# Kernel optimization log

Hardware: AMD Instinct MI355X
Metric: run time of the kernel (lower is better)

## Reference

```python
import jax, jax.numpy as jnp
import numpy as np

B, S, HID = 2, 2048, 2048
H, HKV, D = 16, 8, 128
RQ, RK, RV = 6, 2, 2
WINDOW = 1024
SOFTCAP = 50.0
SCALING = D ** -0.5
NEG_INF = -2.3819763e38  # gemma mask fill value (fp32 safe)


def _rope(x, cos, sin):
    # Gemma rotary: split last dim into two halves treated as (real, imag).
    d2 = x.shape[-1] // 2
    x1, x2 = x[..., :d2], x[..., d2:]
    return jnp.concatenate([x1 * cos - x2 * sin, x1 * sin + x2 * cos], axis=-1)


def setup_inputs() -> dict:
    key = jax.random.key(0)
    ks = jax.random.split(key, 8)
    hidden_states = jax.random.normal(ks[0], (B, S, HID), jnp.float32)
    w = 0.02
    W_A_q = jax.random.normal(ks[1], (HID, H * RQ), jnp.float32) * w
    W_B_q = jax.random.normal(ks[2], (HID, H * RQ * D), jnp.float32) * w
    W_A_k = jax.random.normal(ks[3], (HID, HKV * RK), jnp.float32) * w
    W_B_k = jax.random.normal(ks[4], (HID, RK * D), jnp.float32) * w
    W_A_v = jax.random.normal(ks[5], (HID, HKV * RV), jnp.float32) * w
    W_B_v = jax.random.normal(ks[6], (HID, RV * D), jnp.float32) * w
    W_o = jax.random.normal(ks[7], (H * D, HID), jnp.float32) * w
    # rotary tables (theta=10000)
    pos = jnp.arange(S, dtype=jnp.float32)
    inv = 1.0 / (10000.0 ** (jnp.arange(0, D, 2, dtype=jnp.float32) / D))
    ang = pos[:, None] * inv[None, :]  # [S, D/2]
    freqs_cos, freqs_sin = jnp.cos(ang), jnp.sin(ang)
    # causal + sliding-window additive mask [B,1,S,S]
    i = jnp.arange(S)[:, None]
    j = jnp.arange(S)[None, :]
    allowed = (j <= i) & (i - j < WINDOW)
    mask = jnp.where(allowed, 0.0, NEG_INF).astype(jnp.float32)
    mask = jnp.broadcast_to(mask[None, None], (B, 1, S, S))
    kv_write_indices = jnp.arange(S, dtype=jnp.int32)  # prefill: identity write
    return {
        'hidden_states': hidden_states, 'W_A_q': W_A_q, 'W_B_q': W_B_q,
        'W_A_k': W_A_k, 'W_B_k': W_B_k, 'W_A_v': W_A_v, 'W_B_v': W_B_v,
        'W_o': W_o, 'freqs_cos': freqs_cos, 'freqs_sin': freqs_sin,
        'mask': mask, 'kv_write_indices': kv_write_indices,
    }


def reference(hidden_states, W_A_q, W_B_q, W_A_k, W_B_k, W_A_v, W_B_v, W_o,
              freqs_cos, freqs_sin, mask, kv_write_indices):
    # Prefill: kv_write_indices == arange(S); factorized cache == current factors.
    b, s, _ = hidden_states.shape
    Aq = (hidden_states @ W_A_q).reshape(b, s, H, RQ)       # [b,s,H,Rq]
    Bq = (hidden_states @ W_B_q).reshape(b, s, H, RQ, D)    # [b,s,H,Rq,d]
    Ak = (hidden_states @ W_A_k).reshape(b, s, HKV, RK)
    Bk = (hidden_states @ W_B_k).reshape(b, s, RK, D)
    Av = (hidden_states @ W_A_v).reshape(b, s, HKV, RV)
    Bv = (hidden_states @ W_B_v).reshape(b, s, RV, D)
    # RoPE on the B factors (as in the original: applied to B_q rows and B_k rows)
    Bq = _rope(Bq, freqs_cos[:, None, None, :], freqs_sin[:, None, None, :])
    Bk = _rope(Bk, freqs_cos[:, None, :], freqs_sin[:, None, :])
    # Contract rank factors. Identical math to the per-head
    # einsum('bqrd,bksd->bqkrs') + einsum('bqr,bks,bqkrs->bqk') since the
    # bilinear form factorizes: sum_{r,s} Aq_r Ak_s <Bq_r, Bk_s> = <q, k>.
    q = jnp.einsum('bshr,bshrd->bshd', Aq, Bq)               # [b,s,H,d]
    k = jnp.einsum('bsgr,bsrd->bsgd', Ak, Bk)                # [b,s,Hkv,d]
    v = jnp.einsum('bsgr,bsrd->bsgd', Av, Bv)
    rep = H // HKV
    k = jnp.repeat(k, rep, axis=2)                            # GQA expand
    v = jnp.repeat(v, rep, axis=2)
    scores = jnp.einsum('bqhd,bkhd->bhqk', q, k) * SCALING
    scores = jnp.tanh(scores / SOFTCAP) * SOFTCAP             # logit softcap
    scores = scores + mask                                    # local sliding mask
    probs = jax.nn.softmax(scores, axis=-1)
    out = jnp.einsum('bhqk,bkhd->bqhd', probs, v).reshape(b, s, H * D)
    return out @ W_o
```

## Files before the change

kernel.cpp:

```cpp
#include <hip/hip_runtime.h>
#include <hip/hip_bf16.h>

#define S_LEN 2048
#define HID 2048
#define NB 2
#define NH 16
#define NKV 8
#define DH 128
#define RQ 6
#define KG 2048
#define SCALING 0.08838834764831845f

typedef __attribute__((ext_vector_type(8))) short s16x8;
typedef __attribute__((ext_vector_type(4))) float f32x4;

__device__ __forceinline__ float bf2f(ushort u) {
    union { unsigned int i; float f; } v; v.i = ((unsigned int)u) << 16; return v.f;
}
__device__ __forceinline__ ushort f2bf(float f) {
    __hip_bfloat16 h = __float2bfloat16(f);
    return *reinterpret_cast<ushort*>(&h);
}
__device__ __forceinline__ void g2lds16(const void* g, void* l) {
    __builtin_amdgcn_global_load_lds((const __attribute__((address_space(1))) void*)g,
                                     (__attribute__((address_space(3))) void*)l, 16, 0, 0);
}

__global__ void k_cvt_bf16(const float* __restrict__ in, ushort* __restrict__ out, int n4) {
    int i = blockIdx.x * 256 + threadIdx.x;
    if (i >= n4) return;
    float4 v = ((const float4*)in)[i];
    ushort4 o;
    o.x = f2bf(v.x); o.y = f2bf(v.y); o.z = f2bf(v.z); o.w = f2bf(v.w);
    ((ushort4*)out)[i] = o;
}

__global__ void k_transpose_w(const float* __restrict__ in, ushort* __restrict__ out, int Nin, int rowOff) {
    __shared__ ushort tile[64][66];
    int k0 = blockIdx.x * 64, n0 = blockIdx.y * 64;
    int t = threadIdx.x;
#pragma unroll
    for (int i = 0; i < 16; ++i) {
        int f = t + i * 256; int r = f >> 6, c = f & 63;
        int nn = n0 + c;
        float v = (nn < Nin) ? in[(size_t)(k0 + r) * Nin + nn] : 0.f;
        tile[r][c] = f2bf(v);
    }
    __syncthreads();
#pragma unroll
    for (int i = 0; i < 16; ++i) {
        int f = t + i * 256; int nr = f >> 6, kc = f & 63;
        int nn = n0 + nr;
        if (nn < Nin) out[(size_t)(rowOff + nn) * KG + k0 + kc] = tile[kc][nr];
    }
}

__device__ __forceinline__ void stc(float* p, float v) { *p = v; }
__device__ __forceinline__ void stc(ushort* p, float v) { *p = f2bf(v); }

template<typename OutT>
__global__ __launch_bounds__(256, 2) void k_gemm(const ushort* __restrict__ A,
                                                 const ushort* __restrict__ Bt,
                                                 OutT* __restrict__ C, int ldc) {
    __shared__ ushort lA[128 * 64];
    __shared__ ushort lB[128 * 64];
    const int tid = threadIdx.x;
    const int l = tid & 63, w = tid >> 6;
    const int gx = gridDim.x;
    int flat = blockIdx.y * gx + blockIdx.x;
    const int nwg = gx * gridDim.y;
    if ((nwg & 7) == 0) {
        int qq = nwg >> 3;
        flat = (flat & 7) * qq + (flat >> 3);
    }
    const int m0 = (flat % gx) * 128, n0 = (flat / gx) * 128;
    const int wm = w >> 1, wn = w & 1;
    f32x4 acc[4][4] = {};
    const int swz = 16 * ((tid & 7) ^ ((tid >> 3) & 7));
    const int rowbase = tid >> 3;

    for (int k0 = 0; k0 < KG; k0 += 64) {
#pragma unroll
        for (int i = 0; i < 4; ++i) {
            int row = rowbase + i * 32;
            const char* srcA = (const char*)A + (((size_t)(m0 + row) * KG + k0) * 2) + swz;
            g2lds16(srcA, (char*)lA + tid * 16 + i * 4096);
            const char* srcB = (const char*)Bt + (((size_t)(n0 + row) * KG + k0) * 2) + swz;
            g2lds16(srcB, (char*)lB + tid * 16 + i * 4096);
        }
        __syncthreads();
#pragma unroll
        for (int kk = 0; kk < 2; ++kk) {
            s16x8 af[4], bfr[4];
            const int kb = kk * 64 + (l >> 4) * 16;
#pragma unroll
            for (int mf = 0; mf < 4; ++mf) {
                int row = wm * 64 + mf * 16 + (l & 15);
                af[mf] = *(const s16x8*)((const char*)lA + row * 128 + (kb ^ ((row & 7) << 4)));
            }
#pragma unroll
            for (int nf = 0; nf < 4; ++nf) {
                int row = wn * 64 + nf * 16 + (l & 15);
                bfr[nf] = *(const s16x8*)((const char*)lB + row * 128 + (kb ^ ((row & 7) << 4)));
            }
#pragma unroll
            for (int mf = 0; mf < 4; ++mf)
#pragma unroll
                for (int nf = 0; nf < 4; ++nf)
                    acc[mf][nf] = __builtin_amdgcn_mfma_f32_16x16x32_bf16(af[mf], bfr[nf], acc[mf][nf], 0, 0, 0);
        }
        __syncthreads();
    }
#pragma unroll
    for (int mf = 0; mf < 4; ++mf)
#pragma unroll
        for (int r = 0; r < 4; ++r) {
            int row = m0 + wm * 64 + mf * 16 + (l >> 4) * 4 + r;
#pragma unroll
            for (int nf = 0; nf < 4; ++nf) {
                int col = n0 + wn * 64 + nf * 16 + (l & 15);
                stc(C + (size_t)row * ldc + col, acc[mf][nf][r]);
            }
        }
}

__global__ __launch_bounds__(512, 2) void k_gemm8(const ushort* __restrict__ A,
                                                  const ushort* __restrict__ Bt,
                                                  ushort* __restrict__ C, int ldc) {
    __shared__ char sB[131072];
    const int tid = threadIdx.x;
    const int l = tid & 63, wid = tid >> 6;
    const int wr = wid >> 2, wc = wid & 3;

    int flat = blockIdx.x;
    const int nwg = gridDim.x;
    if ((nwg & 7) == 0) {
        int qq = nwg >> 3;
        flat = (flat & 7) * qq + (flat >> 3);
    }
    const int m0 = (flat & 15) * 256;
    const int n0 = (flat >> 4) * 256;

    const int rb = tid >> 3;
    const int swz = 16 * ((tid & 7) ^ (rb & 7));
    const char* pAh[2][2];
    const char* pBh[2][2];
#pragma unroll
    for (int h = 0; h < 2; ++h)
#pragma unroll
        for (int j = 0; j < 2; ++j) {
            pAh[h][j] = (const char*)A + (size_t)(m0 + j * 128 + h * 64 + rb) * (KG * 2) + swz;
            pBh[h][j] = (const char*)Bt + (size_t)(n0 + (j * 2 + (tid >> 8)) * 64 + h * 32 + (rb & 31)) * (KG * 2) + swz;
        }

    f32x4 acc[8][4] = {};
    s16x8 af[4][2], bf[4][2];

    const int arow = (l & 15) * 128;
    const int kxor0 = (0 * 64 + (l >> 4) * 16) ^ ((l & 7) << 4);
    const int kxor1 = (1 * 64 + (l >> 4) * 16) ^ ((l & 7) << 4);

#define STG_A(T, D, H)                                                                     \
    do {                                                                                   \
        g2lds16(pAh[H][0] + (size_t)(T) * 128, sB + (D) * 65536 + (H) * 16384 + tid * 16); \
        g2lds16(pAh[H][1] + (size_t)(T) * 128, sB + (D) * 65536 + (H) * 16384 + 8192 + tid * 16); \
    } while (0)
#define STG_B(T, D, H)                                                                     \
    do {                                                                                   \
        g2lds16(pBh[H][0] + (size_t)(T) * 128, sB + (D) * 65536 + 32768 + (H) * 16384 + tid * 16); \
        g2lds16(pBh[H][1] + (size_t)(T) * 128, sB + (D) * 65536 + 32768 + (H) * 16384 + 8192 + tid * 16); \
    } while (0)
#define RD_A(D, MH)                                                                        \
    do {                                                                                   \
        const char* ab = sB + (D) * 65536 + (MH) * 16384 + wr * 8192;                      \
        _Pragma("unroll") for (int mi = 0; mi < 4; ++mi) {                                 \
            af[mi][0] = *(const s16x8*)(ab + mi * 2048 + arow + kxor0);                    \
            af[mi][1] = *(const s16x8*)(ab + mi * 2048 + arow + kxor1);                    \
        }                                                                                  \
    } while (0)
#define RD_B(D, BH)                                                                        \
    do {                                                                                   \
        const char* bb = sB + (D) * 65536 + 32768 + (BH) * 16384 + wc * 4096;              \
        _Pragma("unroll") for (int ni = 0; ni < 2; ++ni) {                                 \
            bf[(BH) * 2 + ni][0] = *(const s16x8*)(bb + ni * 2048 + arow + kxor0);         \
            bf[(BH) * 2 + ni][1] = *(const s16x8*)(bb + ni * 2048 + arow + kxor1);         \
        }                                                                                  \
    } while (0)
#define QMFMA(MQ, NQ)                                                                      \
    do {                                                                                   \
        __builtin_amdgcn_s_setprio(1);                                                     \
        _Pragma("unroll") for (int mi = 0; mi < 4; ++mi)                                   \
        _Pragma("unroll") for (int ni = 0; ni < 2; ++ni)                                   \
        _Pragma("unroll") for (int k2 = 0; k2 < 2; ++k2)                                   \
            acc[(MQ) * 4 + mi][(NQ) * 2 + ni] = __builtin_amdgcn_mfma_f32_16x16x32_bf16(   \
                af[mi][k2], bf[(NQ) * 2 + ni][k2], acc[(MQ) * 4 + mi][(NQ) * 2 + ni], 0, 0, 0); \
        __builtin_amdgcn_s_setprio(0);                                                     \
    } while (0)
#define BAR()                                   \
    do {                                        \
        asm volatile("" ::: "memory");          \
        __builtin_amdgcn_s_barrier();           \
        asm volatile("" ::: "memory");          \
    } while (0)
#define VM6() asm volatile("s_waitcnt vmcnt(6)" ::: "memory")
#define VM0() asm volatile("s_waitcnt vmcnt(0)" ::: "memory")

    STG_A(0, 0, 0); STG_A(0, 0, 1); STG_B(0, 0, 0); STG_B(0, 0, 1);
    STG_B(1, 1, 0); STG_B(1, 1, 1); STG_A(1, 1, 0);
    VM6();
    BAR();

    for (int i = 0; i < 16; ++i) {
        const bool last = (i == 15);
        const int t1 = 2 * i + 1, t2 = 2 * i + 2, t3 = 2 * i + 3;
        RD_A(0, 0); RD_B(0, 0);
        STG_A(t1, 1, 1);
        BAR(); QMFMA(0, 0); BAR();
        RD_B(0, 1);
        if (!last) STG_A(t2, 0, 0);
        BAR(); QMFMA(0, 1); BAR();
        RD_A(0, 1);
        if (!last) STG_B(t2, 0, 0);
        BAR(); QMFMA(1, 1); BAR();
        if (!last) { STG_B(t2, 0, 1); VM6(); } else { VM0(); }
        BAR(); QMFMA(1, 0); BAR();
        RD_A(1, 0); RD_B(1, 0);
        if (!last) STG_A(t2, 0, 1);
        BAR(); QMFMA(0, 0); BAR();
        RD_B(1, 1);
        if (!last) STG_B(t3, 1, 0);
        BAR(); QMFMA(0, 1); BAR();
        RD_A(1, 1);
        if (!last) STG_B(t3, 1, 1);
        BAR(); QMFMA(1, 1); BAR();
        if (!last) { STG_A(t3, 1, 0); VM6(); }
        BAR(); QMFMA(1, 0); BAR();
    }

#undef STG_A
#undef STG_B
#undef RD_A
#undef RD_B
#undef QMFMA

#pragma unroll
    for (int mf = 0; mf < 8; ++mf)
#pragma unroll
        for (int r = 0; r < 4; ++r) {
            int row = m0 + wr * 128 + mf * 16 + (l >> 4) * 4 + r;
#pragma unroll
            for (int nf = 0; nf < 4; ++nf) {
                int col = n0 + wc * 64 + nf * 16 + (l & 15);
                C[(size_t)row * ldc + col] = f2bf(acc[mf][nf][r]);
            }
        }
#undef BAR
#undef VM6
#undef VM0
}

__global__ __launch_bounds__(512, 2) void k_gemm8h(const ushort* __restrict__ A,
                                                   const ushort* __restrict__ Bt,
                                                   float* __restrict__ C, int ldc) {
    __shared__ char sB[98304];
    const int tid = threadIdx.x;
    const int l = tid & 63, wid = tid >> 6;
    const int wr = wid >> 2, wc = wid & 3;

    int flat = blockIdx.x;
    const int nwg = gridDim.x;
    if ((nwg & 7) == 0) {
        int qq = nwg >> 3;
        flat = (flat & 7) * qq + (flat >> 3);
    }
    const int m0 = (flat & 31) * 128;
    const int n0 = (flat >> 5) * 256;

    const int rb = tid >> 3;
    const int swz = 16 * ((tid & 7) ^ (rb & 7));
    const char* pA_[2];
    const char* pB_[2][2];
#pragma unroll
    for (int h = 0; h < 2; ++h) {
        pA_[h] = (const char*)A + (size_t)(m0 + (tid >> 8) * 64 + h * 32 + (rb & 31)) * (KG * 2) + swz;
#pragma unroll
        for (int j = 0; j < 2; ++j)
            pB_[h][j] = (const char*)Bt + (size_t)(n0 + (j * 2 + (tid >> 8)) * 64 + h * 32 + (rb & 31)) * (KG * 2) + swz;
    }

    f32x4 acc[4][4] = {};
    s16x8 af[2][2], bf[4][2];

    const int arow = (l & 15) * 128;
    const int kxor0 = ((l >> 4) * 16) ^ ((l & 7) << 4);
    const int kxor1 = (64 + (l >> 4) * 16) ^ ((l & 7) << 4);

#define STG_AH(T, D, H)                                                                    \
    g2lds16(pA_[H] + (size_t)(T) * 128, sB + (D) * 49152 + (H) * 8192 + tid * 16)
#define STG_BH(T, D, H)                                                                    \
    do {                                                                                   \
        g2lds16(pB_[H][0] + (size_t)(T) * 128, sB + (D) * 49152 + 16384 + (H) * 16384 + tid * 16); \
        g2lds16(pB_[H][1] + (size_t)(T) * 128, sB + (D) * 49152 + 16384 + (H) * 16384 + 8192 + tid * 16); \
    } while (0)
#define RD_AH(D, MH)                                                                       \
    do {                                                                                   \
        const char* ab = sB + (D) * 49152 + (MH) * 8192 + wr * 4096;                       \
        _Pragma("unroll") for (int mi = 0; mi < 2; ++mi) {                                 \
            af[mi][0] = *(const s16x8*)(ab + mi * 2048 + arow + kxor0);                    \
            af[mi][1] = *(const s16x8*)(ab + mi * 2048 + arow + kxor1);                    \
        }                                                                                  \
    } while (0)
#define RD_BH(D, BH)                                                                       \
    do {                                                                                   \
        const char* bb = sB + (D) * 49152 + 16384 + (BH) * 16384 + wc * 4096;              \
        _Pragma("unroll") for (int ni = 0; ni < 2; ++ni) {                                 \
            bf[(BH) * 2 + ni][0] = *(const s16x8*)(bb + ni * 2048 + arow + kxor0);         \
            bf[(BH) * 2 + ni][1] = *(const s16x8*)(bb + ni * 2048 + arow + kxor1);         \
        }                                                                                  \
    } while (0)
#define QMFMAH(MQ, NQ)                                                                     \
    do {                                                                                   \
        __builtin_amdgcn_s_setprio(1);                                                     \
        _Pragma("unroll") for (int mi = 0; mi < 2; ++mi)                                   \
        _Pragma("unroll") for (int ni = 0; ni < 2; ++ni)                                   \
        _Pragma("unroll") for (int k2 = 0; k2 < 2; ++k2)                                   \
            acc[(MQ) * 2 + mi][(NQ) * 2 + ni] = __builtin_amdgcn_mfma_f32_16x16x32_bf16(   \
                af[mi][k2], bf[(NQ) * 2 + ni][k2], acc[(MQ) * 2 + mi][(NQ) * 2 + ni], 0, 0, 0); \
        __builtin_amdgcn_s_setprio(0);                                                     \
    } while (0)
#define BAR()                                   \
    do {                                        \
        asm volatile("" ::: "memory");          \
        __builtin_amdgcn_s_barrier();           \
        asm volatile("" ::: "memory");          \
    } while (0)
#define VM5() asm volatile("s_waitcnt vmcnt(5)" ::: "memory")
#define VM0() asm volatile("s_waitcnt vmcnt(0)" ::: "memory")

    STG_AH(0, 0, 0); STG_AH(0, 0, 1); STG_BH(0, 0, 0); STG_BH(0, 0, 1);
    STG_BH(1, 1, 0); STG_BH(1, 1, 1); STG_AH(1, 1, 0);
    VM5();
    BAR();

    for (int i = 0; i < 16; ++i) {
        const bool last = (i == 15);
        const int t1 = 2 * i + 1, t2 = 2 * i + 2, t3 = 2 * i + 3;
        RD_AH(0, 0); RD_BH(0, 0);
        STG_AH(t1, 1, 1);
        BAR(); QMFMAH(0, 0); BAR();
        RD_BH(0, 1);
        if (!last) STG_AH(t2, 0, 0);
        BAR(); QMFMAH(0, 1); BAR();
        RD_AH(0, 1);
        if (!last) STG_BH(t2, 0, 0);
        BAR(); QMFMAH(1, 1); BAR();
        if (!last) { STG_BH(t2, 0, 1); VM5(); } else { VM0(); }
        BAR(); QMFMAH(1, 0); BAR();
        RD_AH(1, 0); RD_BH(1, 0);
        if (!last) STG_AH(t2, 0, 1);
        BAR(); QMFMAH(0, 0); BAR();
        RD_BH(1, 1);
        if (!last) STG_BH(t3, 1, 0);
        BAR(); QMFMAH(0, 1); BAR();
        RD_AH(1, 1);
        if (!last) STG_BH(t3, 1, 1);
        BAR(); QMFMAH(1, 1); BAR();
        if (!last) { STG_AH(t3, 1, 0); VM5(); }
        BAR(); QMFMAH(1, 0); BAR();
    }

#undef STG_AH
#undef STG_BH
#undef RD_AH
#undef RD_BH
#undef QMFMAH
#undef BAR
#undef VM5
#undef VM0

#pragma unroll
    for (int a = 0; a < 4; ++a)
#pragma unroll
        for (int r = 0; r < 4; ++r) {
            int row = m0 + wr * 64 + a * 16 + (l >> 4) * 4 + r;
#pragma unroll
            for (int b2 = 0; b2 < 4; ++b2) {
                int col = n0 + wc * 64 + b2 * 16 + (l & 15);
                C[(size_t)row * ldc + col] = acc[a][b2][r];
            }
        }
}

__global__ void k_contract_q(const ushort* __restrict__ bq, const float* __restrict__ small,
                             const float* __restrict__ cosT, const float* __restrict__ sinT,
                             ushort* __restrict__ q, int pitch, int hbase) {
    int srow = blockIdx.x;
    int b = srow >> 11, sl = srow & 2047;
    int t = threadIdx.x;
    int d2 = t & 63;
    int hloc = blockIdx.y * 4 + (t >> 6);
    int h = hbase + hloc;
    const ushort* bqr = bq + (size_t)srow * pitch + hloc * 768;
    const float* af = small + (size_t)srow * 640 + h * RQ;
    float x1 = 0.f, x2 = 0.f;
#pragma unroll
    for (int r = 0; r < RQ; ++r) {
        float a = af[r];
        x1 += a * bf2f(bqr[r * 128 + d2]);
        x2 += a * bf2f(bqr[r * 128 + 64 + d2]);
    }
    float c = cosT[sl * 64 + d2], s = sinT[sl * 64 + d2];
    float q1 = (x1 * c - x2 * s) * SCALING;
    float q2 = (x1 * s + x2 * c) * SCALING;
    size_t o = ((size_t)(b * NH + h) * S_LEN + sl) * DH + d2;
    q[o] = f2bf(q1);
    q[o + 64] = f2bf(q2);
}

__global__ void k_contract_kv(const float* __restrict__ small, const float* __restrict__ cosT,
                              const float* __restrict__ sinT, ushort* __restrict__ kk,
                              ushort* __restrict__ vT) {
    int srow = blockIdx.x;
    int b = srow >> 11, sl = srow & 2047;
    int t = threadIdx.x;
    int d2 = t & 63, g = t >> 6;
    const float* row = small + (size_t)srow * 640;
    float k1 = 0.f, k2 = 0.f, v1 = 0.f, v2 = 0.f;
#pragma unroll
    for (int r = 0; r < 2; ++r) {
        float ak = row[96 + g * 2 + r];
        k1 += ak * row[128 + r * 128 + d2];
        k2 += ak * row[128 + r * 128 + 64 + d2];
        float av = row[112 + g * 2 + r];
        v1 += av * row[384 + r * 128 + d2];
        v2 += av * row[384 + r * 128 + 64 + d2];
    }
    float c = cosT[sl * 64 + d2], s = sinT[sl * 64 + d2];
    float kr1 = k1 * c - k2 * s, kr2 = k1 * s + k2 * c;
    size_t ko = ((size_t)(b * NKV + g) * S_LEN + sl) * DH + d2;
    kk[ko] = f2bf(kr1);
    kk[ko + 64] = f2bf(kr2);
    size_t vo = ((size_t)(b * NKV + g) * DH + d2) * S_LEN + sl;
    vT[vo] = f2bf(v1);
    vT[vo + (size_t)64 * S_LEN] = f2bf(v2);
}

__global__ __launch_bounds__(512, 2) void k_attn(const ushort* __restrict__ q, const ushort* __restrict__ kk,
                                                 const ushort* __restrict__ vT, ushort* __restrict__ O) {
    __shared__ char sK[16384];
    __shared__ char sV[16384];
    __shared__ char sP[16384];
    const int qb = 31 - blockIdx.x;
    const int bg = blockIdx.y;
    const int b = bg >> 3, g = bg & 7;
    const int tid = threadIdx.x, l = tid & 63, w = tid >> 6;
    const int w4 = w & 3;
    const int h = g * 2 + (w >> 2);
    const int qs = qb * 64;
    const int q0 = qs + w4 * 16;

    const ushort* qbase = q + ((size_t)(b * NH + h) * S_LEN) * DH;
    s16x8 qf[4];
    {
        const char* qrow = (const char*)(qbase + (size_t)(q0 + (l & 15)) * DH);
#pragma unroll
        for (int ds = 0; ds < 4; ++ds)
            qf[ds] = *(const s16x8*)(qrow + ds * 64 + (l >> 4) * 16);
    }
    f32x4 acc[8] = {};
    float lrow[4] = {0.f, 0.f, 0.f, 0.f};

    const size_t kgbase = ((size_t)(b * NKV + g) * S_LEN) * DH * 2;
    const size_t vgbase = ((size_t)(b * NKV + g) * DH) * S_LEN * 2;

    const int jt0 = (qs > 1023) ? ((qs - 1023) >> 6) : 0;
    const int ibase = q0 + (l >> 4) * 4;

    for (int jt = jt0; jt <= qb; ++jt) {
#pragma unroll
        for (int i = 0; i < 2; ++i) {
            int row = (tid >> 4) + i * 32;
            int colb = (tid & 15) * 16;
            const char* src = (const char*)kk + kgbase + ((size_t)(jt * 64 + row)) * 256 + (colb ^ ((row & 7) << 4));
            g2lds16(src, sK + tid * 16 + i * 8192);
        }
#pragma unroll
        for (int i = 0; i < 2; ++i) {
            int row = (tid >> 3) + i * 64;
            int colb = (tid & 7) * 16;
            const char* src = (const char*)vT + vgbase + (size_t)row * 4096 + (size_t)jt * 128 + (colb ^ ((row & 7) << 4));
            g2lds16(src, sV + tid * 16 + i * 8192);
        }
        __syncthreads();

        const bool diag = (jt == qb);
        const bool wclip = (jt == jt0) && (qs > 1023);

        f32x4 sc[4] = {};
#pragma unroll
        for (int ct = 0; ct < 4; ++ct) {
            if (diag && ct > w4) continue;
            f32x4 z = {};
            int row = ct * 16 + (l & 15);
#pragma unroll
            for (int ds = 0; ds < 4; ++ds) {
                int kb = ds * 64 + (l >> 4) * 16;
                s16x8 kf = *(const s16x8*)(sK + row * 256 + (kb ^ ((row & 7) << 4)));
                z = __builtin_amdgcn_mfma_f32_16x16x32_bf16(qf[ds], kf, z, 0, 0, 0);
            }
            sc[ct] = z;
        }
        float p[4][4];
        if (!diag && !wclip) {
#pragma unroll
            for (int ct = 0; ct < 4; ++ct)
#pragma unroll
                for (int r = 0; r < 4; ++r) {
                    float e = __expf(sc[ct][r] * 0.04f);
                    float pe = __expf(-100.f / (e + 1.f));
                    p[ct][r] = pe;
                    lrow[r] += pe;
                }
        } else if (diag) {
#pragma unroll
            for (int ct = 0; ct < 4; ++ct) {
                if (ct > w4) {
#pragma unroll
                    for (int r = 0; r < 4; ++r) p[ct][r] = 0.f;
                    continue;
                }
                int j = jt * 64 + ct * 16 + (l & 15);
#pragma unroll
                for (int r = 0; r < 4; ++r) {
                    float e = __expf(sc[ct][r] * 0.04f);
                    float pe = __expf(-100.f / (e + 1.f));
                    pe = (j <= ibase + r) ? pe : 0.f;
                    p[ct][r] = pe;
                    lrow[r] += pe;
                }
            }
        } else {
#pragma unroll
            for (int ct = 0; ct < 4; ++ct) {
                int j = jt * 64 + ct * 16 + (l & 15);
#pragma unroll
                for (int r = 0; r < 4; ++r) {
                    float e = __expf(sc[ct][r] * 0.04f);
                    float pe = __expf(-100.f / (e + 1.f));
                    pe = (j > ibase + r - 1024) ? pe : 0.f;
                    p[ct][r] = pe;
                    lrow[r] += pe;
                }
            }
        }
#pragma unroll
        for (int ct = 0; ct < 4; ++ct) {
            int col = ct * 16 + (l & 15);
#pragma unroll
            for (int r = 0; r < 4; ++r) {
                int row = (l >> 4) * 4 + r;
                *(ushort*)(sP + w * 2048 + row * 128 + ((col * 2) ^ ((row & 7) << 4))) = f2bf(p[ct][r]);
            }
        }
#pragma unroll
        for (int s2 = 0; s2 < 2; ++s2) {
            int rowp = l & 15;
            int kb = s2 * 64 + (l >> 4) * 16;
            s16x8 pf = *(const s16x8*)(sP + w * 2048 + rowp * 128 + (kb ^ ((rowp & 7) << 4)));
#pragma unroll
            for (int dt = 0; dt < 8; ++dt) {
                int d = dt * 16 + (l & 15);
                s16x8 vf = *(const s16x8*)(sV + d * 128 + (kb ^ ((d & 7) << 4)));
                acc[dt] = __builtin_amdgcn_mfma_f32_16x16x32_bf16(pf, vf, acc[dt], 0, 0, 0);
            }
        }
        __syncthreads();
    }
#pragma unroll
    for (int r = 0; r < 4; ++r) {
        float rs = lrow[r];
        rs += __shfl_xor(rs, 1); rs += __shfl_xor(rs, 2);
        rs += __shfl_xor(rs, 4); rs += __shfl_xor(rs, 8);
        lrow[r] = rs;
    }
#pragma unroll
    for (int r = 0; r < 4; ++r) {
        int row = qs + w4 * 16 + (l >> 4) * 4 + r;
        float inv = 1.f / lrow[r];
#pragma unroll
        for (int dt = 0; dt < 8; ++dt)
            O[((size_t)(b * S_LEN + row)) * HID + h * DH + dt * 16 + (l & 15)] = f2bf(acc[dt][r] * inv);
    }
}

extern "C" void kernel_launch(void* const* d_in, const int* in_sizes, int n_in,
                              void* d_out, int out_size, void* d_ws, size_t ws_size,
                              hipStream_t stream) {
    (void)in_sizes; (void)n_in; (void)out_size;
    const float* hs  = (const float*)d_in[0];
    const float* WAq = (const float*)d_in[1];
    const float* WBq = (const float*)d_in[2];
    const float* WAk = (const float*)d_in[3];
    const float* WBk = (const float*)d_in[4];
    const float* WAv = (const float*)d_in[5];
    const float* WBv = (const float*)d_in[6];
    const float* Wo  = (const float*)d_in[7];
    const float* fc  = (const float*)d_in[8];
    const float* fs  = (const float*)d_in[9];

    char* ws = (char*)d_ws;
    ushort* Xb    = (ushort*)(ws + 0);
    ushort* WtS   = (ushort*)(ws + 16777216);
    ushort* WtBq  = (ushort*)(ws + 19398656);
    ushort* WtWo  = (ushort*)(ws + 69730304);
    float*  Small = (float*) (ws + 78118912);
    ushort* BqC   = (ushort*)(ws + 88604672);

    const bool bigws = (ws_size >= 239599616ull);
    size_t tail = bigws ? 189267968ull : 113770496ull;
    ushort* qB  = (ushort*)(ws + tail);
    ushort* kB  = (ushort*)(ws + tail + 16777216);
    ushort* vTB = (ushort*)(ws + tail + 25165824);
    ushort* OB  = (ushort*)(ws + tail + 33554432);

    k_cvt_bf16<<<8192, 256, 0, stream>>>(hs, Xb, 2097152);
    k_transpose_w<<<dim3(32, 2),   256, 0, stream>>>(WAq, WtS, 96, 0);
    k_transpose_w<<<dim3(32, 1),   256, 0, stream>>>(WAk, WtS, 16, 96);
    k_transpose_w<<<dim3(32, 1),   256, 0, stream>>>(WAv, WtS, 16, 112);
    k_transpose_w<<<dim3(32, 4),   256, 0, stream>>>(WBk, WtS, 256, 128);
    k_transpose_w<<<dim3(32, 4),   256, 0, stream>>>(WBv, WtS, 256, 384);
    k_transpose_w<<<dim3(32, 192), 256, 0, stream>>>(WBq, WtBq, 12288, 0);
    k_transpose_w<<<dim3(32, 32),  256, 0, stream>>>(Wo, WtWo, 2048, 0);

    k_gemm<float><<<dim3(32, 5), 256, 0, stream>>>(Xb, WtS, Small, 640);
    k_contract_kv<<<4096, 512, 0, stream>>>(Small, fc, fs, kB, vTB);

    if (bigws) {
        k_gemm8<<<768, 512, 0, stream>>>(Xb, WtBq, BqC, 12288);
        k_contract_q<<<dim3(4096, 4), 256, 0, stream>>>(BqC, Small, fc, fs, qB, 12288, 0);
    } else {
        for (int c = 0; c < 4; ++c) {
            k_gemm8<<<192, 512, 0, stream>>>(Xb, WtBq + (size_t)c * 3072 * KG, BqC, 3072);
            k_contract_q<<<dim3(4096, 1), 256, 0, stream>>>(BqC, Small, fc, fs, qB, 3072, c * 4);
        }
    }

    k_attn<<<dim3(32, 16), 512, 0, stream>>>(qB, kB, vTB, OB);

    k_gemm8h<<<256, 512, 0, stream>>>(OB, WtWo, (float*)d_out, 2048);
}
```

Before: 499.3 us.

## Double-buffer MFMA fragments in GEMM and vectorize transpose and Q contraction

```diff
diff --git a/kernel.cpp b/kernel.cpp
--- a/kernel.cpp
+++ b/kernel.cpp
@@ -36,22 +36,34 @@
 }
 
 __global__ void k_transpose_w(const float* __restrict__ in, ushort* __restrict__ out, int Nin, int rowOff) {
-    __shared__ ushort tile[64][66];
+    __shared__ ushort tile[64][68];
     int k0 = blockIdx.x * 64, n0 = blockIdx.y * 64;
     int t = threadIdx.x;
 #pragma unroll
-    for (int i = 0; i < 16; ++i) {
-        int f = t + i * 256; int r = f >> 6, c = f & 63;
+    for (int i = 0; i < 4; ++i) {
+        int f = t + i * 256;
+        int r = f >> 4;
+        int c = (f & 15) * 4;
         int nn = n0 + c;
-        float v = (nn < Nin) ? in[(size_t)(k0 + r) * Nin + nn] : 0.f;
-        tile[r][c] = f2bf(v);
+        float4 v = make_float4(0.f, 0.f, 0.f, 0.f);
+        if (nn < Nin) v = *(const float4*)&in[(size_t)(k0 + r) * Nin + nn];
+        ushort4 u;
+        u.x = f2bf(v.x); u.y = f2bf(v.y); u.z = f2bf(v.z); u.w = f2bf(v.w);
+        *(ushort4*)&tile[r][c] = u;
     }
     __syncthreads();
 #pragma unroll
-    for (int i = 0; i < 16; ++i) {
-        int f = t + i * 256; int nr = f >> 6, kc = f & 63;
+    for (int i = 0; i < 4; ++i) {
+        int f = t + i * 256;
+        int nr = f >> 4;
+        int kc = (f & 15) * 4;
         int nn = n0 + nr;
-        if (nn < Nin) out[(size_t)(rowOff + nn) * KG + k0 + kc] = tile[kc][nr];
+        if (nn < Nin) {
+            ushort4 u;
+            u.x = tile[kc][nr]; u.y = tile[kc + 1][nr];
+            u.z = tile[kc + 2][nr]; u.w = tile[kc + 3][nr];
+            *(ushort4*)&out[(size_t)(rowOff + nn) * KG + k0 + kc] = u;
+        }
     }
 }
 
@@ -154,7 +166,9 @@
         }
 
     f32x4 acc[8][4] = {};
-    s16x8 af[4][2], bf[4][2];
+    s16x8 afA[4][2], afB[4][2];
+    s16x8 bf0a[2][2], bf0b[2][2];
+    s16x8 bf1[2][2];
 
     const int arow = (l & 15) * 128;
     const int kxor0 = (0 * 64 + (l >> 4) * 16) ^ ((l & 7) << 4);
@@ -170,30 +184,30 @@
         g2lds16(pBh[H][0] + (size_t)(T) * 128, sB + (D) * 65536 + 32768 + (H) * 16384 + tid * 16); \
         g2lds16(pBh[H][1] + (size_t)(T) * 128, sB + (D) * 65536 + 32768 + (H) * 16384 + 8192 + tid * 16); \
     } while (0)
-#define RD_A(D, MH)                                                                        \
+#define RD_A2(D, MH, DST)                                                                  \
     do {                                                                                   \
         const char* ab = sB + (D) * 65536 + (MH) * 16384 + wr * 8192;                      \
         _Pragma("unroll") for (int mi = 0; mi < 4; ++mi) {                                 \
-            af[mi][0] = *(const s16x8*)(ab + mi * 2048 + arow + kxor0);                    \
-            af[mi][1] = *(const s16x8*)(ab + mi * 2048 + arow + kxor1);                    \
+            DST[mi][0] = *(const s16x8*)(ab + mi * 2048 + arow + kxor0);                   \
+            DST[mi][1] = *(const s16x8*)(ab + mi * 2048 + arow + kxor1);                   \
         }                                                                                  \
     } while (0)
-#define RD_B(D, BH)                                                                        \
+#define RD_B2(D, BH, DST)                                                                  \
     do {                                                                                   \
         const char* bb = sB + (D) * 65536 + 32768 + (BH) * 16384 + wc * 4096;              \
         _Pragma("unroll") for (int ni = 0; ni < 2; ++ni) {                                 \
-            bf[(BH) * 2 + ni][0] = *(const s16x8*)(bb + ni * 2048 + arow + kxor0);         \
-            bf[(BH) * 2 + ni][1] = *(const s16x8*)(bb + ni * 2048 + arow + kxor1);         \
+            DST[ni][0] = *(const s16x8*)(bb + ni * 2048 + arow + kxor0);                   \
+            DST[ni][1] = *(const s16x8*)(bb + ni * 2048 + arow + kxor1);                   \
         }                                                                                  \
     } while (0)
-#define QMFMA(MQ, NQ)                                                                      \
+#define QMFMA2(MQ, NQ, AF, BF)                                                             \
     do {                                                                                   \
         __builtin_amdgcn_s_setprio(1);                                                     \
         _Pragma("unroll") for (int mi = 0; mi < 4; ++mi)                                   \
         _Pragma("unroll") for (int ni = 0; ni < 2; ++ni)                                   \
         _Pragma("unroll") for (int k2 = 0; k2 < 2; ++k2)                                   \
             acc[(MQ) * 4 + mi][(NQ) * 2 + ni] = __builtin_amdgcn_mfma_f32_16x16x32_bf16(   \
-                af[mi][k2], bf[(NQ) * 2 + ni][k2], acc[(MQ) * 4 + mi][(NQ) * 2 + ni], 0, 0, 0); \
+                AF[mi][k2], BF[ni][k2], acc[(MQ) * 4 + mi][(NQ) * 2 + ni], 0, 0, 0);       \
         __builtin_amdgcn_s_setprio(0);                                                     \
     } while (0)
 #define BAR()                                   \
@@ -209,39 +223,47 @@
     STG_B(1, 1, 0); STG_B(1, 1, 1); STG_A(1, 1, 0);
     VM6();
     BAR();
+    RD_A2(0, 0, afA);
+    RD_B2(0, 0, bf0a);
 
     for (int i = 0; i < 16; ++i) {
         const bool last = (i == 15);
         const int t1 = 2 * i + 1, t2 = 2 * i + 2, t3 = 2 * i + 3;
-        RD_A(0, 0); RD_B(0, 0);
+        RD_B2(0, 1, bf1);
+        RD_A2(0, 1, afB);
         STG_A(t1, 1, 1);
-        BAR(); QMFMA(0, 0); BAR();
-        RD_B(0, 1);
+        BAR(); QMFMA2(0, 0, afA, bf0a); BAR();
         if (!last) STG_A(t2, 0, 0);
-        BAR(); QMFMA(0, 1); BAR();
-        RD_A(0, 1);
+        BAR(); QMFMA2(0, 1, afA, bf1); BAR();
         if (!last) STG_B(t2, 0, 0);
-        BAR(); QMFMA(1, 1); BAR();
+        BAR(); QMFMA2(1, 1, afB, bf1); BAR();
         if (!last) { STG_B(t2, 0, 1); VM6(); } else { VM0(); }
-        BAR(); QMFMA(1, 0); BAR();
-        RD_A(1, 0); RD_B(1, 0);
+        BAR();
+        RD_A2(1, 0, afA);
+        RD_B2(1, 0, bf0b);
+        QMFMA2(1, 0, afB, bf0a); BAR();
+        RD_B2(1, 1, bf1);
+        RD_A2(1, 1, afB);
         if (!last) STG_A(t2, 0, 1);
-        BAR(); QMFMA(0, 0); BAR();
-        RD_B(1, 1);
+        BAR(); QMFMA2(0, 0, afA, bf0b); BAR();
         if (!last) STG_B(t3, 1, 0);
-        BAR(); QMFMA(0, 1); BAR();
-        RD_A(1, 1);
+        BAR(); QMFMA2(0, 1, afA, bf1); BAR();
         if (!last) STG_B(t3, 1, 1);
-        BAR(); QMFMA(1, 1); BAR();
+        BAR(); QMFMA2(1, 1, afB, bf1); BAR();
         if (!last) { STG_A(t3, 1, 0); VM6(); }
-        BAR(); QMFMA(1, 0); BAR();
+        BAR();
+        if (!last) { RD_A2(0, 0, afA); RD_B2(0, 0, bf0a); }
+        QMFMA2(1, 0, afB, bf0b); BAR();
     }
 
 #undef STG_A
 #undef STG_B
-#undef RD_A
-#undef RD_B
-#undef QMFMA
+#undef RD_A2
+#undef RD_B2
+#undef QMFMA2
+#undef BAR
+#undef VM6
+#undef VM0
 
 #pragma unroll
     for (int mf = 0; mf < 8; ++mf)
@@ -254,9 +276,6 @@
                 C[(size_t)row * ldc + col] = f2bf(acc[mf][nf][r]);
             }
         }
-#undef BAR
-#undef VM6
-#undef VM0
 }
 
 __global__ __launch_bounds__(512, 2) void k_gemm8h(const ushort* __restrict__ A,
@@ -397,24 +416,35 @@
     int srow = blockIdx.x;
     int b = srow >> 11, sl = srow & 2047;
     int t = threadIdx.x;
-    int d2 = t & 63;
+    int l = t & 63;
     int hloc = blockIdx.y * 4 + (t >> 6);
     int h = hbase + hloc;
     const ushort* bqr = bq + (size_t)srow * pitch + hloc * 768;
     const float* af = small + (size_t)srow * 640 + h * RQ;
-    float x1 = 0.f, x2 = 0.f;
+    float y0 = 0.f, y1 = 0.f;
 #pragma unroll
     for (int r = 0; r < RQ; ++r) {
         float a = af[r];
-        x1 += a * bf2f(bqr[r * 128 + d2]);
-        x2 += a * bf2f(bqr[r * 128 + 64 + d2]);
-    }
-    float c = cosT[sl * 64 + d2], s = sinT[sl * 64 + d2];
-    float q1 = (x1 * c - x2 * s) * SCALING;
-    float q2 = (x1 * s + x2 * c) * SCALING;
-    size_t o = ((size_t)(b * NH + h) * S_LEN + sl) * DH + d2;
-    q[o] = f2bf(q1);
-    q[o + 64] = f2bf(q2);
+        ushort2 v = *(const ushort2*)&bqr[r * 128 + 2 * l];
+        y0 += a * bf2f(v.x);
+        y1 += a * bf2f(v.y);
+    }
+    float z0 = __shfl_xor(y0, 32);
+    float z1 = __shfl_xor(y1, 32);
+    int d = (l & 31) * 2;
+    float2 cs = *(const float2*)&cosT[sl * 64 + d];
+    float2 sn = *(const float2*)&sinT[sl * 64 + d];
+    size_t o = ((size_t)(b * NH + h) * S_LEN + sl) * DH;
+    ushort2 outv;
+    if (l < 32) {
+        outv.x = f2bf((y0 * cs.x - z0 * sn.x) * SCALING);
+        outv.y = f2bf((y1 * cs.y - z1 * sn.y) * SCALING);
+        *(ushort2*)&q[o + d] = outv;
+    } else {
+        outv.x = f2bf((z0 * sn.x + y0 * cs.x) * SCALING);
+        outv.y = f2bf((z1 * sn.y + y1 * cs.y) * SCALING);
+        *(ushort2*)&q[o + 64 + d] = outv;
+    }
 }
 
 __global__ void k_contract_kv(const float* __restrict__ small, const float* __restrict__ cosT,
```

Result: slower. 555.7 us (+11.3%).
